# Kernel tuning notes

Measured on AMD Instinct MI355X. Metric: run time of the kernel, lower is better.

## Reference

```python
import jax, jax.numpy as jnp
import numpy as np

B, C, H, W, NH = 4, 96, 256, 256, 4


def setup_inputs() -> dict:
    key = jax.random.key(0)
    ks = jax.random.split(key, 8)
    s = 0.05  # keep pre-activations well-scaled
    return {
        "x": jax.random.normal(ks[0], (B, C, H, W), jnp.float32),
        "ff": jax.random.normal(ks[1], (B, C, H, W), jnp.float32),
        "w_q": jax.random.normal(ks[2], (C, C, 1, 1), jnp.float32) * s,
        "w_kv": jax.random.normal(ks[3], (2 * C, C, 1, 1), jnp.float32) * s,
        "w_q_dw": jax.random.normal(ks[4], (C, 1, 3, 3), jnp.float32) * s,
        "w_kv_dw": jax.random.normal(ks[5], (2 * C, 1, 3, 3), jnp.float32) * s,
        "w_out": jax.random.normal(ks[6], (C, C, 1, 1), jnp.float32) * s,
        "temperature": jnp.ones((NH, 1, 1), jnp.float32),
    }


def _conv1x1(x, w):
    # pointwise conv == channel GEMM; w: [O, I, 1, 1]
    return jnp.einsum('bchw,oc->bohw', x, w[:, :, 0, 0])


def _dwconv3(x, w):
    # depthwise 3x3, padding=1; w: [C, 1, 3, 3]
    return jax.lax.conv_general_dilated(
        x, w, window_strides=(1, 1), padding='SAME',
        feature_group_count=x.shape[1],
        dimension_numbers=('NCHW', 'OIHW', 'NCHW'))


def _l2norm(t, eps=1e-12):
    # L2-normalize along last (HW) axis, torch F.normalize semantics
    n = jnp.sqrt(jnp.sum(t * t, axis=-1, keepdims=True))
    return t / jnp.maximum(n, eps)


def reference(x, ff, w_q, w_kv, w_q_dw, w_kv_dw, w_out, temperature):
    b, c, h, w = x.shape
    q = _dwconv3(_conv1x1(ff, w_q), w_q_dw)          # [B,C,H,W]
    kv = _dwconv3(_conv1x1(x, w_kv), w_kv_dw)        # [B,2C,H,W]
    k, v = jnp.split(kv, 2, axis=1)

    def heads(t):
        return t.reshape(b, NH, c // NH, h * w)       # [B,nh,c,HW]

    q = _l2norm(heads(q))
    k = _l2norm(heads(k))
    v = heads(v)
    # channel-wise (transposed) attention: [B,nh,c,c]
    attn = jax.nn.softmax(jnp.einsum('bhcn,bhdn->bhcd', q, k) * temperature, axis=-1)
    o = jnp.einsum('bhcd,bhdn->bhcn', attn, v).reshape(b, c, h, w)
    return _conv1x1(o, w_out)
```

## Files before the change

### kernel.cpp

```cpp
#include <hip/hip_runtime.h>
#include <hip/hip_bf16.h>
#include <hip/hip_fp16.h>

typedef unsigned int u32;
typedef unsigned short u16;
typedef _Float16 f16;

static constexpr int HWn = 65536;

typedef __attribute__((ext_vector_type(8))) f16 f16x8;
typedef __attribute__((ext_vector_type(4))) float f32x4;

__device__ __forceinline__ float h2f(u16 u) {
    union { u16 s; f16 h; } z; z.s = u; return (float)z.h;
}
__device__ __forceinline__ u16 f2h(float f) {
    union { u16 s; f16 h; } z; z.h = (f16)f; return z.s;
}
__device__ __forceinline__ u32 pack2h(float a, float b) {
    union { u32 i; f16 h[2]; } z; z.h[0] = (f16)a; z.h[1] = (f16)b; return z.i;
}
__device__ __forceinline__ float hlo(u32 u) {
    union { u32 i; f16 h[2]; } z; z.i = u; return (float)z.h[0];
}
__device__ __forceinline__ float hhi(u32 u) {
    union { u32 i; f16 h[2]; } z; z.i = u; return (float)z.h[1];
}
__device__ __forceinline__ float sq2h(u32 a) {
    const float l = hlo(a), h = hhi(a);
    return fmaf(l, l, h * h);
}

__device__ __forceinline__ int xoff(int px, int icb) {
    return px * 128 + (((icb ^ (px & 7) ^ ((px >> 3) & 7))) << 3);
}

__global__ __launch_bounds__(256) void k_prep_w(
    const float* __restrict__ wq, const float* __restrict__ wkv,
    u16* __restrict__ wf)
{
    const int i = blockIdx.x * 256 + threadIdx.x;
    if (i >= 288 * 96) return;
    const int row = i / 96, ic = i % 96;
    const float w = (row < 96) ? wq[row * 96 + ic] : wkv[(row - 96) * 96 + ic];
    wf[i] = f2h(w);
}

__global__ __launch_bounds__(256, 5) void k_conv_mfma(
    const float* __restrict__ ff, const float* __restrict__ x,
    const u16* __restrict__ wf,
    u16* __restrict__ qpre, u16* __restrict__ kvpre)
{
    const int b = blockIdx.z, sec = blockIdx.y;
    const int px0 = blockIdx.x * 128;
    const int tid = threadIdx.x;

    __shared__ __align__(16) u16 xs[16384];

    const float* src = (sec == 0 ? ff : x) + (size_t)b * 96 * HWn;

    const int icq = (tid >> 4) * 2;
    const int pxs = (tid & 15) * 8;
    #pragma unroll 1
    for (int p = 0; p < 3; ++p) {
        const int ic = p * 32 + icq;
        const float* rp0 = src + (size_t)ic * HWn + px0 + pxs;
        const float* rp1 = rp0 + HWn;
        const float4 a0 = *reinterpret_cast<const float4*>(rp0);
        const float4 a1 = *reinterpret_cast<const float4*>(rp0 + 4);
        const float4 b0 = *reinterpret_cast<const float4*>(rp1);
        const float4 b1 = *reinterpret_cast<const float4*>(rp1 + 4);
        const int icb = ic >> 3, icl = ic & 7;
        const float e0[8] = {a0.x, a0.y, a0.z, a0.w, a1.x, a1.y, a1.z, a1.w};
        const float e1[8] = {b0.x, b0.y, b0.z, b0.w, b1.x, b1.y, b1.z, b1.w};
        #pragma unroll
        for (int j = 0; j < 8; ++j) {
            const int o = xoff(pxs + j, icb) + icl;
            *reinterpret_cast<u32*>(&xs[o]) = pack2h(e0[j], e1[j]);
        }
    }
    __syncthreads();

    const int lane = tid & 63;
    const int wv = tid >> 6;
    const int oc0 = (wv >> 1) * 48;
    const int pxw = (wv & 1) * 64;
    const int lr = lane & 15, lg = lane >> 4;

    const int npass = (sec == 0) ? 1 : 2;
    #pragma unroll 1
    for (int kvs = 0; kvs < npass; ++kvs) {
        const u16* wh = wf + ((sec == 0) ? 0 : (96 + kvs * 96)) * 96;
        u16* dst = (sec == 0) ? (qpre + (size_t)b * 96 * HWn)
                              : (kvpre + (size_t)b * 192 * HWn + (size_t)kvs * 96 * HWn);

        f32x4 acc[3][4];
        #pragma unroll
        for (int m = 0; m < 3; ++m)
            #pragma unroll
            for (int n = 0; n < 4; ++n)
                acc[m][n] = (f32x4){0.f, 0.f, 0.f, 0.f};

        #pragma unroll 1
        for (int kt = 0; kt < 3; ++kt) {
            const int kb = kt * 32;
            f16x8 B[4];
            #pragma unroll
            for (int n = 0; n < 4; ++n)
                B[n] = *(const f16x8*)(xs + xoff(pxw + n * 16 + lr, (kb >> 3) + lg));
            f16x8 A[3];
            #pragma unroll
            for (int m = 0; m < 3; ++m)
                A[m] = *(const f16x8*)(wh + (oc0 + m * 16 + lr) * 96 + kb + lg * 8);
            #pragma unroll
            for (int m = 0; m < 3; ++m)
                #pragma unroll
                for (int n = 0; n < 4; ++n)
                    acc[m][n] = __builtin_amdgcn_mfma_f32_16x16x32_f16(A[m], B[n], acc[m][n], 0, 0, 0);
        }

        #pragma unroll
        for (int m = 0; m < 3; ++m) {
            #pragma unroll
            for (int i = 0; i < 4; ++i) {
                const int oc = oc0 + m * 16 + lg * 4 + i;
                u16* drow = dst + (size_t)oc * HWn + px0;
                #pragma unroll
                for (int n = 0; n < 4; ++n)
                    drow[pxw + n * 16 + lr] = f2h(acc[m][n][i]);
            }
        }
    }
}

__global__ __launch_bounds__(512) void k_dw_fused(
    const u16* __restrict__ qpre, const u16* __restrict__ kvpre,
    const float* __restrict__ wqdw, const float* __restrict__ wkvdw,
    u16* __restrict__ vout, float* __restrict__ ssq, float* __restrict__ Sg)
{
    const int bid = blockIdx.x;
    const int wg = (bid & 7) * 256 + (bid >> 3);
    const int b = wg >> 9;
    const int rem = wg & 511;
    const int y = rem >> 1;
    const int tx = (rem & 1) * 128;
    const int tid = threadIdx.x;
    const int lane = tid & 63;
    const int chunk = tid & 15;
    const int x0l = chunk * 8;
    const int xg = tx + x0l;

    __shared__ __align__(16) u16 qs[96][136];
    __shared__ __align__(16) u16 ks[96][136];

    #pragma unroll 1
    for (int it = 0; it < 9; ++it) {
        const int p = it * 32 + (tid >> 4);
        const u16* src; const float* wp; int c;
        if (p < 96)       { c = p;       src = qpre  + ((size_t)(b * 96 + c)) * HWn;       wp = wqdw  + c * 9; }
        else if (p < 192) { c = p - 96;  src = kvpre + ((size_t)(b * 192 + c)) * HWn;      wp = wkvdw + c * 9; }
        else              { c = p - 192; src = kvpre + ((size_t)(b * 192 + 96 + c)) * HWn; wp = wkvdw + (96 + c) * 9; }

        float a0 = 0.f, a1 = 0.f, a2 = 0.f, a3 = 0.f, a4 = 0.f, a5 = 0.f, a6 = 0.f, a7 = 0.f;

        #pragma unroll
        for (int r = 0; r < 3; ++r) {
            const int ry = y + r - 1;
            if ((unsigned)ry < 256u) {
                const u16* row = src + ry * 256 + xg;
                const uint4 m = *reinterpret_cast<const uint4*>(row);
                const float v1 = hlo(m.x), v2 = hhi(m.x);
                const float v3 = hlo(m.y), v4 = hhi(m.y);
                const float v5 = hlo(m.z), v6 = hhi(m.z);
                const float v7 = hlo(m.w), v8 = hhi(m.w);
                const float lv = __shfl(v8, (lane - 1) & 63);
                const float rv = __shfl(v1, (lane + 1) & 63);
                const float v0 = (chunk == 0)  ? ((xg > 0)       ? h2f(row[-1]) : 0.f) : lv;
                const float v9 = (chunk == 15) ? ((xg + 8 < 256) ? h2f(row[8])  : 0.f) : rv;
                const float w0 = wp[r * 3 + 0], w1 = wp[r * 3 + 1], w2 = wp[r * 3 + 2];
                a0 = fmaf(w0, v0, fmaf(w1, v1, fmaf(w2, v2, a0)));
                a1 = fmaf(w0, v1, fmaf(w1, v2, fmaf(w2, v3, a1)));
                a2 = fmaf(w0, v2, fmaf(w1, v3, fmaf(w2, v4, a2)));
                a3 = fmaf(w0, v3, fmaf(w1, v4, fmaf(w2, v5, a3)));
                a4 = fmaf(w0, v4, fmaf(w1, v5, fmaf(w2, v6, a4)));
                a5 = fmaf(w0, v5, fmaf(w1, v6, fmaf(w2, v7, a5)));
                a6 = fmaf(w0, v6, fmaf(w1, v7, fmaf(w2, v8, a6)));
                a7 = fmaf(w0, v7, fmaf(w1, v8, fmaf(w2, v9, a7)));
            }
        }

        const uint4 o = make_uint4(pack2h(a0, a1), pack2h(a2, a3), pack2h(a4, a5), pack2h(a6, a7));
        if (p < 96) {
            *reinterpret_cast<uint4*>(&qs[c][x0l]) = o;
        } else if (p < 192) {
            *reinterpret_cast<uint4*>(&ks[c][x0l]) = o;
        } else {
            *reinterpret_cast<uint4*>(vout + ((size_t)(b * 96 + c)) * HWn + y * 256 + xg) = o;
        }
    }
    __syncthreads();

    if (tid < 384) {
        const int half = tid >= 192;
        const int r = tid - half * 192;
        const uint4* rr = reinterpret_cast<const uint4*>(
            (r < 96 ? &qs[r][0] : &ks[r - 96][0]) + half * 64);
        float s = 0.f;
        #pragma unroll
        for (int pch = 0; pch < 8; ++pch) {
            const uint4 a = rr[pch];
            s += sq2h(a.x) + sq2h(a.y) + sq2h(a.z) + sq2h(a.w);
        }
        atomicAdd(ssq + b * 192 + r, s);
    }

    {
        const int w = tid >> 6;
        const int h = w & 3, mt = w >> 2;
        const int lr2 = lane & 15, lg2 = lane >> 4;
        const int ar = h * 24 + min(mt * 16 + lr2, 23);
        f32x4 acc2[2];
        acc2[0] = (f32x4){0.f, 0.f, 0.f, 0.f};
        acc2[1] = (f32x4){0.f, 0.f, 0.f, 0.f};
        #pragma unroll
        for (int ks4 = 0; ks4 < 4; ++ks4) {
            const f16x8 A = *(const f16x8*)(&qs[ar][ks4 * 32 + lg2 * 8]);
            #pragma unroll
            for (int nt = 0; nt < 2; ++nt) {
                const int bc = h * 24 + min(nt * 16 + lr2, 23);
                const f16x8 B = *(const f16x8*)(&ks[bc][ks4 * 32 + lg2 * 8]);
                acc2[nt] = __builtin_amdgcn_mfma_f32_16x16x32_f16(A, B, acc2[nt], 0, 0, 0);
            }
        }
        #pragma unroll
        for (int nt = 0; nt < 2; ++nt) {
            const int col = nt * 16 + lr2;
            #pragma unroll
            for (int reg = 0; reg < 4; ++reg) {
                const int row24 = mt * 16 + lg2 * 4 + reg;
                if (row24 < 24 && col < 24)
                    atomicAdd(Sg + b * 2304 + h * 576 + row24 * 24 + col, acc2[nt][reg]);
            }
        }
    }
}

__global__ __launch_bounds__(256) void k_attn_fold(
    const float* __restrict__ ssq, const float* __restrict__ S,
    const float* __restrict__ temp, const float* __restrict__ w_out,
    u16* __restrict__ mf)
{
    const int b = blockIdx.x;
    const int tid = threadIdx.x;
    __shared__ float rq[96], rk[96], att[2304];

    if (tid < 96) {
        rq[tid] = 1.f / fmaxf(sqrtf(ssq[b * 192 + tid]), 1e-12f);
    } else if (tid < 192) {
        const int c = tid - 96;
        rk[c] = 1.f / fmaxf(sqrtf(ssq[b * 192 + 96 + c]), 1e-12f);
    }
    __syncthreads();

    if (tid < 96) {
        const int h = tid / 24, i = tid % 24;
        const float tmp = temp[h];
        const float rqi = rq[h * 24 + i];
        float l[24];
        float m = -1e30f;
        #pragma unroll
        for (int j = 0; j < 24; ++j) {
            l[j] = S[b * 2304 + (h * 24 + i) * 24 + j] * rqi * rk[h * 24 + j] * tmp;
            m = fmaxf(m, l[j]);
        }
        float ssum = 0.f;
        #pragma unroll
        for (int j = 0; j < 24; ++j) { l[j] = expf(l[j] - m); ssum += l[j]; }
        const float inv = 1.f / ssum;
        #pragma unroll
        for (int j = 0; j < 24; ++j) att[(h * 24 + i) * 24 + j] = l[j] * inv;
    }
    __syncthreads();

    for (int k = 0; k < 36; ++k) {
        const int id = k * 256 + tid;
        const int dg = id / 96, oc = id % 96;
        const int h = dg / 24, d24 = dg % 24;
        float s = 0.f;
        #pragma unroll
        for (int i = 0; i < 24; ++i) {
            s += w_out[oc * 96 + h * 24 + i] * att[(h * 24 + i) * 24 + d24];
        }
        mf[b * 9216 + oc * 96 + dg] = f2h(s);
    }
}

__global__ __launch_bounds__(256, 5) void k_out_mfma(
    const u16* __restrict__ v, const u16* __restrict__ mf,
    float* __restrict__ out)
{
    const int b = blockIdx.y;
    const int px0 = blockIdx.x * 128;
    const int tid = threadIdx.x;
    __shared__ __align__(16) u16 xt[16384];

    const u16* vb = v + (size_t)b * 96 * HWn;
    const u16* mh = mf + b * 9216;

    const int icq = (tid >> 4) * 2;
    const int pxs = (tid & 15) * 8;
    #pragma unroll 1
    for (int p = 0; p < 3; ++p) {
        const int dg = p * 32 + icq;
        const uint4 u0 = *reinterpret_cast<const uint4*>(vb + (size_t)dg * HWn + px0 + pxs);
        const uint4 u1 = *reinterpret_cast<const uint4*>(vb + (size_t)(dg + 1) * HWn + px0 + pxs);
        const u32 w0[4] = {u0.x, u0.y, u0.z, u0.w};
        const u32 w1[4] = {u1.x, u1.y, u1.z, u1.w};
        const int icb = dg >> 3, icl = dg & 7;
        #pragma unroll
        for (int j = 0; j < 8; ++j) {
            const u32 lo = (w0[j >> 1] >> ((j & 1) * 16)) & 0xffffu;
            const u32 hi = (w1[j >> 1] >> ((j & 1) * 16)) & 0xffffu;
            const int o = xoff(pxs + j, icb) + icl;
            *reinterpret_cast<u32*>(&xt[o]) = (hi << 16) | lo;
        }
    }
    __syncthreads();

    const int lane = tid & 63;
    const int wv = tid >> 6;
    const int oc0 = (wv >> 1) * 48;
    const int pxw = (wv & 1) * 64;
    const int lr = lane & 15, lg = lane >> 4;

    f32x4 acc[3][4];
    #pragma unroll
    for (int m = 0; m < 3; ++m)
        #pragma unroll
        for (int n = 0; n < 4; ++n)
            acc[m][n] = (f32x4){0.f, 0.f, 0.f, 0.f};

    #pragma unroll 1
    for (int kt = 0; kt < 3; ++kt) {
        const int kb = kt * 32;
        f16x8 B[4];
        #pragma unroll
        for (int n = 0; n < 4; ++n)
            B[n] = *(const f16x8*)(xt + xoff(pxw + n * 16 + lr, (kb >> 3) + lg));
        f16x8 A[3];
        #pragma unroll
        for (int m = 0; m < 3; ++m)
            A[m] = *(const f16x8*)(mh + (oc0 + m * 16 + lr) * 96 + kb + lg * 8);
        #pragma unroll
        for (int m = 0; m < 3; ++m)
            #pragma unroll
            for (int n = 0; n < 4; ++n)
                acc[m][n] = __builtin_amdgcn_mfma_f32_16x16x32_f16(A[m], B[n], acc[m][n], 0, 0, 0);
    }

    #pragma unroll
    for (int m = 0; m < 3; ++m) {
        #pragma unroll
        for (int i = 0; i < 4; ++i) {
            const int oc = oc0 + m * 16 + lg * 4 + i;
            float* drow = out + ((size_t)(b * 96 + oc)) * HWn + px0;
            #pragma unroll
            for (int n = 0; n < 4; ++n)
                drow[pxw + n * 16 + lr] = acc[m][n][i];
        }
    }
}

extern "C" void kernel_launch(void* const* d_in, const int* in_sizes, int n_in,
                              void* d_out, int out_size, void* d_ws, size_t ws_size,
                              hipStream_t stream) {
    (void)in_sizes; (void)n_in; (void)out_size; (void)ws_size;
    const float* x      = (const float*)d_in[0];
    const float* ff     = (const float*)d_in[1];
    const float* w_q    = (const float*)d_in[2];
    const float* w_kv   = (const float*)d_in[3];
    const float* w_q_dw = (const float*)d_in[4];
    const float* w_kv_dw= (const float*)d_in[5];
    const float* w_out  = (const float*)d_in[6];
    const float* temp   = (const float*)d_in[7];
    float* out = (float*)d_out;

    char* ws = (char*)d_ws;
    u16* qpre   = (u16*)(ws);
    u16* kvpre  = (u16*)(ws + 50331648);
    u16* vbuf   = (u16*)(ws + 150994944);
    float* ssq  = (float*)(ws + 201326592);
    float* S    = (float*)(ws + 201329664);
    u16* wf     = (u16*)(ws + 201366528);
    u16* mf     = (u16*)(ws + 201421824);

    hipMemsetAsync(ssq, 0, 3072 + 36864, stream);

    k_prep_w<<<108, 256, 0, stream>>>(w_q, w_kv, wf);
    k_conv_mfma<<<dim3(512, 2, 4), 256, 0, stream>>>(ff, x, wf, qpre, kvpre);
    k_dw_fused<<<dim3(2048), 512, 0, stream>>>(qpre, kvpre, w_q_dw, w_kv_dw, vbuf, ssq, S);
    k_attn_fold<<<4, 256, 0, stream>>>(ssq, S, temp, w_out, mf);
    k_out_mfma<<<dim3(512, 4), 256, 0, stream>>>(vbuf, mf, out);
}
```

Baseline: 275.4 us.

## Split depthwise conv into q/k and v kernels with prefetch and packed fdot2

The fused depthwise kernel is split in two. One kernel computes q/k rows into shared memory for the norms and the Gram matrix. A separate kernel handles v with full 256-wide rows per block, so it needs no edge gathers. Both kernels double-buffer the next channel's three row loads and compute the 3x3 taps with packed half-precision fdot2 on 16-bit shifted pairs instead of scalar fp32 FMAs. The costs are an extra launch, more register pressure from prefetch buffers, and accumulation through f16 dot products.

```diff
diff --git a/kernel.cpp b/kernel.cpp
--- a/kernel.cpp
+++ b/kernel.cpp
@@ -9,6 +9,7 @@
 static constexpr int HWn = 65536;
 
 typedef __attribute__((ext_vector_type(8))) f16 f16x8;
+typedef __attribute__((ext_vector_type(2))) f16 f16x2;
 typedef __attribute__((ext_vector_type(4))) float f32x4;
 
 __device__ __forceinline__ float h2f(u16 u) {
@@ -29,6 +30,20 @@
 __device__ __forceinline__ float sq2h(u32 a) {
     const float l = hlo(a), h = hhi(a);
     return fmaf(l, l, h * h);
+}
+
+#if defined(__has_builtin)
+#if __has_builtin(__builtin_amdgcn_fdot2)
+#define HAS_FDOT2 1
+#endif
+#endif
+__device__ __forceinline__ float fdot2a(u32 a, u32 b, float c) {
+#ifdef HAS_FDOT2
+    union { u32 i; f16x2 h; } A, B; A.i = a; B.i = b;
+    return __builtin_amdgcn_fdot2(A.h, B.h, c, false);
+#else
+    return fmaf(hlo(a), hlo(b), fmaf(hhi(a), hhi(b), c));
+#endif
 }
 
 __device__ __forceinline__ int xoff(int px, int icb) {
@@ -133,10 +148,29 @@
     }
 }
 
-__global__ __launch_bounds__(512) void k_dw_fused(
+__device__ __forceinline__ void row3tap(
+    const uint4 m, u32 lv, u32 rv, u32 w01, u32 w2z, float* a)
+{
+    const u32 P0 = m.x, P1 = m.y, P2 = m.z, P3 = m.w;
+    const u32 s0 = (lv >> 16) | (P0 << 16);
+    const u32 s1 = (P0 >> 16) | (P1 << 16);
+    const u32 s2 = (P1 >> 16) | (P2 << 16);
+    const u32 s3 = (P2 >> 16) | (P3 << 16);
+    const u32 s4 = (P3 >> 16) | (rv << 16);
+    a[0] = fdot2a(w2z, s1, fdot2a(w01, s0, a[0]));
+    a[1] = fdot2a(w2z, P1, fdot2a(w01, P0, a[1]));
+    a[2] = fdot2a(w2z, s2, fdot2a(w01, s1, a[2]));
+    a[3] = fdot2a(w2z, P2, fdot2a(w01, P1, a[3]));
+    a[4] = fdot2a(w2z, s3, fdot2a(w01, s2, a[4]));
+    a[5] = fdot2a(w2z, P3, fdot2a(w01, P2, a[5]));
+    a[6] = fdot2a(w2z, s4, fdot2a(w01, s3, a[6]));
+    a[7] = fdot2a(w2z, rv, fdot2a(w01, P3, a[7]));
+}
+
+__global__ __launch_bounds__(512) void k_dw_qk(
     const u16* __restrict__ qpre, const u16* __restrict__ kvpre,
     const float* __restrict__ wqdw, const float* __restrict__ wkvdw,
-    u16* __restrict__ vout, float* __restrict__ ssq, float* __restrict__ Sg)
+    float* __restrict__ ssq, float* __restrict__ Sg)
 {
     const int bid = blockIdx.x;
     const int wg = (bid & 7) * 256 + (bid >> 3);
@@ -146,56 +180,71 @@
     const int tx = (rem & 1) * 128;
     const int tid = threadIdx.x;
     const int lane = tid & 63;
+    const int pq = tid >> 4;
     const int chunk = tid & 15;
     const int x0l = chunk * 8;
     const int xg = tx + x0l;
 
+    const bool vr0 = (y > 0), vr2 = (y < 255);
+    const bool le = (chunk == 0) && (xg > 0);
+    const bool re = (chunk == 15) && (xg + 8 < 256);
+
     __shared__ __align__(16) u16 qs[96][136];
     __shared__ __align__(16) u16 ks[96][136];
 
+    auto addr = [&](int it, const u16*& src, const float*& wp, int& c, int& seg) {
+        const int p = it * 32 + pq;
+        if (p < 96) { c = p;      src = qpre  + ((size_t)(b * 96 + c)) * HWn;  wp = wqdw  + c * 9; seg = 0; }
+        else        { c = p - 96; src = kvpre + ((size_t)(b * 192 + c)) * HWn; wp = wkvdw + c * 9; seg = 1; }
+    };
+    auto issue = [&](const u16* src, uint4* m, u32* el, u32* er) {
+        const uint4 z = make_uint4(0u, 0u, 0u, 0u);
+        const u16* r0 = src + (y - 1) * 256 + xg;
+        const u16* r1 = r0 + 256;
+        const u16* r2 = r1 + 256;
+        m[0] = vr0 ? *reinterpret_cast<const uint4*>(r0) : z;
+        m[1] = *reinterpret_cast<const uint4*>(r1);
+        m[2] = vr2 ? *reinterpret_cast<const uint4*>(r2) : z;
+        el[0] = (le && vr0) ? ((u32)r0[-1] << 16) : 0u;  er[0] = (re && vr0) ? (u32)r0[8] : 0u;
+        el[1] = le ? ((u32)r1[-1] << 16) : 0u;           er[1] = re ? (u32)r1[8] : 0u;
+        el[2] = (le && vr2) ? ((u32)r2[-1] << 16) : 0u;  er[2] = (re && vr2) ? (u32)r2[8] : 0u;
+    };
+
+    const u16* srcC; const float* wpC; int cC, segC;
+    addr(0, srcC, wpC, cC, segC);
+    uint4 mcur[3]; u32 elc[3], erc[3];
+    issue(srcC, mcur, elc, erc);
+
     #pragma unroll 1
-    for (int it = 0; it < 9; ++it) {
-        const int p = it * 32 + (tid >> 4);
-        const u16* src; const float* wp; int c;
-        if (p < 96)       { c = p;       src = qpre  + ((size_t)(b * 96 + c)) * HWn;       wp = wqdw  + c * 9; }
-        else if (p < 192) { c = p - 96;  src = kvpre + ((size_t)(b * 192 + c)) * HWn;      wp = wkvdw + c * 9; }
-        else              { c = p - 192; src = kvpre + ((size_t)(b * 192 + 96 + c)) * HWn; wp = wkvdw + (96 + c) * 9; }
-
-        float a0 = 0.f, a1 = 0.f, a2 = 0.f, a3 = 0.f, a4 = 0.f, a5 = 0.f, a6 = 0.f, a7 = 0.f;
-
+    for (int it = 0; it < 6; ++it) {
+        const u16* srcN; const float* wpN; int cN, segN;
+        uint4 mnx[3]; u32 eln[3], ern[3];
+        if (it < 5) {
+            addr(it + 1, srcN, wpN, cN, segN);
+            issue(srcN, mnx, eln, ern);
+        }
+
+        float a[8] = {0.f, 0.f, 0.f, 0.f, 0.f, 0.f, 0.f, 0.f};
         #pragma unroll
         for (int r = 0; r < 3; ++r) {
-            const int ry = y + r - 1;
-            if ((unsigned)ry < 256u) {
-                const u16* row = src + ry * 256 + xg;
-                const uint4 m = *reinterpret_cast<const uint4*>(row);
-                const float v1 = hlo(m.x), v2 = hhi(m.x);
-                const float v3 = hlo(m.y), v4 = hhi(m.y);
-                const float v5 = hlo(m.z), v6 = hhi(m.z);
-                const float v7 = hlo(m.w), v8 = hhi(m.w);
-                const float lv = __shfl(v8, (lane - 1) & 63);
-                const float rv = __shfl(v1, (lane + 1) & 63);
-                const float v0 = (chunk == 0)  ? ((xg > 0)       ? h2f(row[-1]) : 0.f) : lv;
-                const float v9 = (chunk == 15) ? ((xg + 8 < 256) ? h2f(row[8])  : 0.f) : rv;
-                const float w0 = wp[r * 3 + 0], w1 = wp[r * 3 + 1], w2 = wp[r * 3 + 2];
-                a0 = fmaf(w0, v0, fmaf(w1, v1, fmaf(w2, v2, a0)));
-                a1 = fmaf(w0, v1, fmaf(w1, v2, fmaf(w2, v3, a1)));
-                a2 = fmaf(w0, v2, fmaf(w1, v3, fmaf(w2, v4, a2)));
-                a3 = fmaf(w0, v3, fmaf(w1, v4, fmaf(w2, v5, a3)));
-                a4 = fmaf(w0, v4, fmaf(w1, v5, fmaf(w2, v6, a4)));
-                a5 = fmaf(w0, v5, fmaf(w1, v6, fmaf(w2, v7, a5)));
-                a6 = fmaf(w0, v6, fmaf(w1, v7, fmaf(w2, v8, a6)));
-                a7 = fmaf(w0, v7, fmaf(w1, v8, fmaf(w2, v9, a7)));
-            }
-        }
-
-        const uint4 o = make_uint4(pack2h(a0, a1), pack2h(a2, a3), pack2h(a4, a5), pack2h(a6, a7));
-        if (p < 96) {
-            *reinterpret_cast<uint4*>(&qs[c][x0l]) = o;
-        } else if (p < 192) {
-            *reinterpret_cast<uint4*>(&ks[c][x0l]) = o;
-        } else {
-            *reinterpret_cast<uint4*>(vout + ((size_t)(b * 96 + c)) * HWn + y * 256 + xg) = o;
+            const u32 w01 = pack2h(wpC[r * 3 + 0], wpC[r * 3 + 1]);
+            const u32 w2z = pack2h(wpC[r * 3 + 2], 0.f);
+            const u32 lvn = __shfl((int)mcur[r].w, (lane - 1) & 63);
+            const u32 rvn = __shfl((int)mcur[r].x, (lane + 1) & 63);
+            const u32 lv = (chunk == 0)  ? elc[r] : lvn;
+            const u32 rv = (chunk == 15) ? erc[r] : rvn;
+            row3tap(mcur[r], lv, rv, w01, w2z, a);
+        }
+
+        const uint4 o = make_uint4(pack2h(a[0], a[1]), pack2h(a[2], a[3]),
+                                   pack2h(a[4], a[5]), pack2h(a[6], a[7]));
+        if (segC == 0) *reinterpret_cast<uint4*>(&qs[cC][x0l]) = o;
+        else           *reinterpret_cast<uint4*>(&ks[cC][x0l]) = o;
+
+        if (it < 5) {
+            #pragma unroll
+            for (int r = 0; r < 3; ++r) { mcur[r] = mnx[r]; elc[r] = eln[r]; erc[r] = ern[r]; }
+            wpC = wpN; cC = cN; segC = segN;
         }
     }
     __syncthreads();
@@ -241,6 +290,65 @@
                 if (row24 < 24 && col < 24)
                     atomicAdd(Sg + b * 2304 + h * 576 + row24 * 24 + col, acc2[nt][reg]);
             }
+        }
+    }
+}
+
+__global__ __launch_bounds__(512) void k_dw_v(
+    const u16* __restrict__ kvpre, const float* __restrict__ wkvdw,
+    u16* __restrict__ vout)
+{
+    const int bid = blockIdx.x;
+    const int y = (bid & 7) * 32 + (bid >> 3);
+    const int b = blockIdx.y;
+    const int tid = threadIdx.x;
+    const int lane = tid & 63;
+    const int pl = tid >> 5;
+    const int chunk = tid & 31;
+    const int x0 = chunk * 8;
+
+    const bool vr0 = (y > 0), vr2 = (y < 255);
+
+    auto issue = [&](int it, uint4* m) {
+        const int c = it * 16 + pl;
+        const u16* src = kvpre + ((size_t)(b * 192 + 96 + c)) * HWn;
+        const uint4 z = make_uint4(0u, 0u, 0u, 0u);
+        const u16* r0 = src + (y - 1) * 256 + x0;
+        m[0] = vr0 ? *reinterpret_cast<const uint4*>(r0) : z;
+        m[1] = *reinterpret_cast<const uint4*>(r0 + 256);
+        m[2] = vr2 ? *reinterpret_cast<const uint4*>(r0 + 512) : z;
+    };
+
+    uint4 mcur[3];
+    issue(0, mcur);
+
+    #pragma unroll 1
+    for (int it = 0; it < 6; ++it) {
+        uint4 mnx[3];
+        if (it < 5) issue(it + 1, mnx);
+
+        const int c = it * 16 + pl;
+        const float* wp = wkvdw + (96 + c) * 9;
+
+        float a[8] = {0.f, 0.f, 0.f, 0.f, 0.f, 0.f, 0.f, 0.f};
+        #pragma unroll
+        for (int r = 0; r < 3; ++r) {
+            const u32 w01 = pack2h(wp[r * 3 + 0], wp[r * 3 + 1]);
+            const u32 w2z = pack2h(wp[r * 3 + 2], 0.f);
+            const u32 lvn = __shfl((int)mcur[r].w, (lane - 1) & 63);
+            const u32 rvn = __shfl((int)mcur[r].x, (lane + 1) & 63);
+            const u32 lv = (chunk == 0)  ? 0u : lvn;
+            const u32 rv = (chunk == 31) ? 0u : rvn;
+            row3tap(mcur[r], lv, rv, w01, w2z, a);
+        }
+
+        const uint4 o = make_uint4(pack2h(a[0], a[1]), pack2h(a[2], a[3]),
+                                   pack2h(a[4], a[5]), pack2h(a[6], a[7]));
+        *reinterpret_cast<uint4*>(vout + ((size_t)(b * 96 + c)) * HWn + y * 256 + x0) = o;
+
+        if (it < 5) {
+            #pragma unroll
+            for (int r = 0; r < 3; ++r) mcur[r] = mnx[r];
         }
     }
 }
@@ -394,11 +502,12 @@
     u16* wf     = (u16*)(ws + 201366528);
     u16* mf     = (u16*)(ws + 201421824);
 
-    hipMemsetAsync(ssq, 0, 3072 + 36864, stream);
+    hipMemsetAsync(ws + 201326592, 0, 3072 + 36864, stream);
 
     k_prep_w<<<108, 256, 0, stream>>>(w_q, w_kv, wf);
     k_conv_mfma<<<dim3(512, 2, 4), 256, 0, stream>>>(ff, x, wf, qpre, kvpre);
-    k_dw_fused<<<dim3(2048), 512, 0, stream>>>(qpre, kvpre, w_q_dw, w_kv_dw, vbuf, ssq, S);
+    k_dw_qk<<<dim3(2048), 512, 0, stream>>>(qpre, kvpre, w_q_dw, w_kv_dw, ssq, S);
+    k_dw_v<<<dim3(256, 4), 512, 0, stream>>>(kvpre, w_kv_dw, vbuf);
     k_attn_fold<<<4, 256, 0, stream>>>(ssq, S, temp, w_out, mf);
     k_out_mfma<<<dim3(512, 4), 256, 0, stream>>>(vbuf, mf, out);
 }
```

New measurement: 273.0 us. About the same (-0.9%).
